# Kernel tuning notes

Hardware: AMD Instinct MI355X
Metric: run time of the kernel (lower is better)

The kernel has to match this reference:

```python
import jax, jax.numpy as jnp
import numpy as np

INV_SQRT2 = 0.7071067811865476
SCALES = 3


def dwt_analysis(x, dec_lo, dec_hi, scales):
    """Multi-level 1D DWT along last axis (pywt/ptwt convention).
    x: [B, D]. dec_lo/dec_hi are cross-correlation filters (torch conv1d
    semantics, i.e. the flipped pywt decomposition filters as stored by the
    repo). Returns [cA_s | cD_s | ... | cD_1] truncated to the last D columns
    (identity for Haar on power-of-two D)."""
    flen = dec_lo.shape[0]
    pad = (2 * flen - 3) // 2  # ptwt zero-pad; 0 for Haar (flen=2)
    filt = jnp.stack([dec_lo, dec_hi])[:, None, :]  # [2, 1, flen]
    lo = x[:, None, :]  # [B, 1, D]
    highs = []
    for _ in range(scales):
        out = jax.lax.conv_general_dilated(
            lo, filt, window_strides=(2,), padding=[(pad, pad)],
            dimension_numbers=('NCH', 'OIH', 'NCH'))  # [B, 2, D/2]
        lo = out[:, 0:1, :]
        highs.append(out[:, 1, :])
    coeffs = jnp.concatenate([lo[:, 0, :]] + highs[::-1], axis=-1)
    return coeffs[:, -x.shape[-1]:]


def setup_inputs() -> dict:
    key = jax.random.key(0)
    k1, k2, k3, k4, k5 = jax.random.split(key, 5)
    B, D = 4096, 4096
    x = jax.random.normal(k1, (B, D), jnp.float32)
    diag_s = jax.random.normal(k2, (D,), jnp.float32)
    diag_g = jax.random.normal(k3, (D,), jnp.float32)
    diag_b = jax.random.normal(k4, (D,), jnp.float32)
    perm = jax.random.permutation(k5, jnp.arange(D))  # random column permutation
    # Haar analysis filters in cross-correlation (torch conv1d) orientation
    dec_lo = jnp.array([INV_SQRT2, INV_SQRT2], jnp.float32)
    dec_hi = jnp.array([INV_SQRT2, -INV_SQRT2], jnp.float32)
    return {"x": x, "diag_s": diag_s, "diag_g": diag_g, "diag_b": diag_b,
            "dec_lo": dec_lo, "dec_hi": dec_hi, "perm": perm, "scales": SCALES}


def reference(x, diag_s, diag_g, diag_b, dec_lo, dec_hi, perm, scales):
    # mul_b: x @ diag(b) == columnwise scale (same math, no O(d^2) matmul)
    h = x * diag_b
    h = dwt_analysis(h, dec_lo, dec_hi, scales)
    # mul_p: x @ P for a permutation matrix == column gather
    h = jnp.take(h, perm, axis=1)
    h = h * diag_g  # mul_g
    h = dwt_analysis(h, dec_lo, dec_hi, scales)
    return h * diag_s  # mul_s
```

## Files before the change

### kernel.cpp

```cpp
#include <hip/hip_runtime.h>


#define D   4096
#define NT  256
#define R   4

#define C_INV_SQRT2 0.70710678118654752440f

typedef float vf2 __attribute__((ext_vector_type(2)));
typedef float vf4 __attribute__((ext_vector_type(4)));

static __device__ __forceinline__ int swz(int i) {
    return i ^ ((i >> 5) & 31);
}

static __device__ __forceinline__ void dwt3_reg(const float v[16],
                                                float a3[2], float d3[2],
                                                float d2[4], float d1[8]) {
    float a1[8];
    #pragma unroll
    for (int j = 0; j < 8; ++j) {
        a1[j] = (v[2 * j] + v[2 * j + 1]) * C_INV_SQRT2;
        d1[j] = (v[2 * j] - v[2 * j + 1]) * C_INV_SQRT2;
    }
    float a2[4];
    #pragma unroll
    for (int j = 0; j < 4; ++j) {
        a2[j] = (a1[2 * j] + a1[2 * j + 1]) * C_INV_SQRT2;
        d2[j] = (a1[2 * j] - a1[2 * j + 1]) * C_INV_SQRT2;
    }
    #pragma unroll
    for (int j = 0; j < 2; ++j) {
        a3[j] = (a2[2 * j] + a2[2 * j + 1]) * C_INV_SQRT2;
        d3[j] = (a2[2 * j] - a2[2 * j + 1]) * C_INV_SQRT2;
    }
}

__global__ __launch_bounds__(NT) void wavelet_rows_kernel(
    const float* __restrict__ x,
    const float* __restrict__ diag_s,
    const float* __restrict__ diag_g,
    const float* __restrict__ diag_b,
    const int*   __restrict__ perm,
    float*       __restrict__ out)
{
    __shared__ float buf[D];

    const int t = threadIdx.x;
    const size_t row0 = (size_t)blockIdx.x * R;

    float db[16], dg[16];
    int   pidx[16];
    {
        const vf4* b4 = (const vf4*)diag_b;
        const vf4* g4 = (const vf4*)diag_g;
        const int4* p4 = (const int4*)perm;
        #pragma unroll
        for (int k = 0; k < 4; ++k) {
            vf4 bv = b4[4 * t + k];
            db[4 * k + 0] = bv.x; db[4 * k + 1] = bv.y;
            db[4 * k + 2] = bv.z; db[4 * k + 3] = bv.w;
            vf4 gv = g4[4 * t + k];
            dg[4 * k + 0] = gv.x; dg[4 * k + 1] = gv.y;
            dg[4 * k + 2] = gv.z; dg[4 * k + 3] = gv.w;
            int4 pv = p4[4 * t + k];
            pidx[4 * k + 0] = pv.x; pidx[4 * k + 1] = pv.y;
            pidx[4 * k + 2] = pv.z; pidx[4 * k + 3] = pv.w;
        }
    }

    vf4 xv[4];
    {
        const vf4* x4 = (const vf4*)(x + row0 * (size_t)D);
        #pragma unroll
        for (int k = 0; k < 4; ++k) xv[k] = x4[4 * t + k];
    }

    for (int r = 0; r < R; ++r) {
        float v[16];
        #pragma unroll
        for (int k = 0; k < 4; ++k) {
            v[4 * k + 0] = xv[k].x * db[4 * k + 0];
            v[4 * k + 1] = xv[k].y * db[4 * k + 1];
            v[4 * k + 2] = xv[k].z * db[4 * k + 2];
            v[4 * k + 3] = xv[k].w * db[4 * k + 3];
        }

        if (r + 1 < R) {
            const vf4* xn = (const vf4*)(x + (row0 + r + 1) * (size_t)D);
            #pragma unroll
            for (int k = 0; k < 4; ++k) xv[k] = xn[4 * t + k];
        }

        float a3[2], d3[2], d2[4], d1[8];
        dwt3_reg(v, a3, d3, d2, d1);

        #pragma unroll
        for (int j = 0; j < 2; ++j) buf[swz(2 * t + j)]        = a3[j];
        #pragma unroll
        for (int j = 0; j < 2; ++j) buf[swz(512 + 2 * t + j)]  = d3[j];
        #pragma unroll
        for (int j = 0; j < 4; ++j) buf[swz(1024 + 4 * t + j)] = d2[j];
        #pragma unroll
        for (int j = 0; j < 8; ++j) buf[swz(2048 + 8 * t + j)] = d1[j];

        __syncthreads();

        float w[16];
        #pragma unroll
        for (int k = 0; k < 16; ++k) {
            w[k] = buf[swz(pidx[k])] * dg[k];
        }

        __syncthreads();

        float b3[2], e3[2], e2[4], e1[8];
        dwt3_reg(w, b3, e3, e2, e1);

        float* orow = out + (row0 + r) * (size_t)D;
        {
            const vf2* s2 = (const vf2*)diag_s;
            vf2* o2 = (vf2*)orow;
            vf2 sv, ov;
            sv = s2[t];
            ov.x = b3[0] * sv.x; ov.y = b3[1] * sv.y;
            o2[t] = ov;
            sv = s2[256 + t];
            ov.x = e3[0] * sv.x; ov.y = e3[1] * sv.y;
            o2[256 + t] = ov;

            const vf4* s4 = (const vf4*)diag_s;
            vf4* o4 = (vf4*)orow;
            vf4 sw, o;
            sw = s4[256 + t];
            o.x = e2[0] * sw.x; o.y = e2[1] * sw.y;
            o.z = e2[2] * sw.z; o.w = e2[3] * sw.w;
            o4[256 + t] = o;
            sw = s4[512 + 2 * t];
            o.x = e1[0] * sw.x; o.y = e1[1] * sw.y;
            o.z = e1[2] * sw.z; o.w = e1[3] * sw.w;
            o4[512 + 2 * t] = o;
            sw = s4[512 + 2 * t + 1];
            o.x = e1[4] * sw.x; o.y = e1[5] * sw.y;
            o.z = e1[6] * sw.z; o.w = e1[7] * sw.w;
            o4[512 + 2 * t + 1] = o;
        }
    }
}

extern "C" void kernel_launch(void* const* d_in, const int* in_sizes, int n_in,
                              void* d_out, int out_size, void* d_ws, size_t ws_size,
                              hipStream_t stream) {
    const float* x      = (const float*)d_in[0];
    const float* diag_s = (const float*)d_in[1];
    const float* diag_g = (const float*)d_in[2];
    const float* diag_b = (const float*)d_in[3];
    const int* perm     = (const int*)d_in[6];
    float* out          = (float*)d_out;

    const int B = 4096 / R;
    wavelet_rows_kernel<<<B, NT, 0, stream>>>(x, diag_s, diag_g, diag_b, perm, out);
}
```

Baseline: 131.7 us.

## Interleave four rows per LDS slot as vf4 to batch the permutation gather

Each block now loads all four rows up front and runs the first DWT on every row. It then stores the coefficients interleaved as one vf4 per column in a 64 KB LDS array, so the permutation gather becomes one 16-byte LDS read per column for all four rows. This replaces four per-row rounds of scalar LDS writes and gathers, and their eight barriers, with a single barrier. The cost is much higher register pressure from holding 4x16 values plus the inputs, and 64 KB of LDS per block, which limits occupancy. The swizzle is changed to suit 16-byte elements.

```diff
diff --git a/kernel.cpp b/kernel.cpp
--- a/kernel.cpp
+++ b/kernel.cpp
@@ -10,29 +10,27 @@
 typedef float vf2 __attribute__((ext_vector_type(2)));
 typedef float vf4 __attribute__((ext_vector_type(4)));
 
-static __device__ __forceinline__ int swz(int i) {
-    return i ^ ((i >> 5) & 31);
+static __device__ __forceinline__ int swzB(int p) {
+    return p ^ ((p >> 3) & 7);
 }
 
-static __device__ __forceinline__ void dwt3_reg(const float v[16],
-                                                float a3[2], float d3[2],
-                                                float d2[4], float d1[8]) {
+static __device__ __forceinline__ void dwt3_reg(const float v[16], float c[16]) {
     float a1[8];
     #pragma unroll
     for (int j = 0; j < 8; ++j) {
-        a1[j] = (v[2 * j] + v[2 * j + 1]) * C_INV_SQRT2;
-        d1[j] = (v[2 * j] - v[2 * j + 1]) * C_INV_SQRT2;
+        a1[j]     = (v[2 * j] + v[2 * j + 1]) * C_INV_SQRT2;
+        c[8 + j]  = (v[2 * j] - v[2 * j + 1]) * C_INV_SQRT2;
     }
     float a2[4];
     #pragma unroll
     for (int j = 0; j < 4; ++j) {
-        a2[j] = (a1[2 * j] + a1[2 * j + 1]) * C_INV_SQRT2;
-        d2[j] = (a1[2 * j] - a1[2 * j + 1]) * C_INV_SQRT2;
+        a2[j]    = (a1[2 * j] + a1[2 * j + 1]) * C_INV_SQRT2;
+        c[4 + j] = (a1[2 * j] - a1[2 * j + 1]) * C_INV_SQRT2;
     }
     #pragma unroll
     for (int j = 0; j < 2; ++j) {
-        a3[j] = (a2[2 * j] + a2[2 * j + 1]) * C_INV_SQRT2;
-        d3[j] = (a2[2 * j] - a2[2 * j + 1]) * C_INV_SQRT2;
+        c[j]     = (a2[2 * j] + a2[2 * j + 1]) * C_INV_SQRT2;
+        c[2 + j] = (a2[2 * j] - a2[2 * j + 1]) * C_INV_SQRT2;
     }
 }
 
@@ -44,7 +42,7 @@
     const int*   __restrict__ perm,
     float*       __restrict__ out)
 {
-    __shared__ float buf[D];
+    __shared__ vf4 lds4[D];
 
     const int t = threadIdx.x;
     const size_t row0 = (size_t)blockIdx.x * R;
@@ -69,82 +67,89 @@
         }
     }
 
-    vf4 xv[4];
-    {
-        const vf4* x4 = (const vf4*)(x + row0 * (size_t)D);
+    int pos[16];
+    #pragma unroll
+    for (int j = 0; j < 2; ++j) pos[j]     = 2 * t + j;
+    #pragma unroll
+    for (int j = 0; j < 2; ++j) pos[2 + j] = 512 + 2 * t + j;
+    #pragma unroll
+    for (int j = 0; j < 4; ++j) pos[4 + j] = 1024 + 4 * t + j;
+    #pragma unroll
+    for (int j = 0; j < 8; ++j) pos[8 + j] = 2048 + 8 * t + j;
+
+    vf4 xv[R][4];
+    #pragma unroll
+    for (int r = 0; r < R; ++r) {
+        const vf4* x4 = (const vf4*)(x + (row0 + r) * (size_t)D);
         #pragma unroll
-        for (int k = 0; k < 4; ++k) xv[k] = x4[4 * t + k];
+        for (int k = 0; k < 4; ++k) xv[r][k] = x4[4 * t + k];
     }
 
+    float cf[R][16];
+    #pragma unroll
     for (int r = 0; r < R; ++r) {
         float v[16];
         #pragma unroll
         for (int k = 0; k < 4; ++k) {
-            v[4 * k + 0] = xv[k].x * db[4 * k + 0];
-            v[4 * k + 1] = xv[k].y * db[4 * k + 1];
-            v[4 * k + 2] = xv[k].z * db[4 * k + 2];
-            v[4 * k + 3] = xv[k].w * db[4 * k + 3];
+            v[4 * k + 0] = xv[r][k].x * db[4 * k + 0];
+            v[4 * k + 1] = xv[r][k].y * db[4 * k + 1];
+            v[4 * k + 2] = xv[r][k].z * db[4 * k + 2];
+            v[4 * k + 3] = xv[r][k].w * db[4 * k + 3];
         }
+        dwt3_reg(v, cf[r]);
+    }
 
-        if (r + 1 < R) {
-            const vf4* xn = (const vf4*)(x + (row0 + r + 1) * (size_t)D);
-            #pragma unroll
-            for (int k = 0; k < 4; ++k) xv[k] = xn[4 * t + k];
-        }
+    #pragma unroll
+    for (int k = 0; k < 16; ++k) {
+        vf4 c4;
+        c4.x = cf[0][k]; c4.y = cf[1][k];
+        c4.z = cf[2][k]; c4.w = cf[3][k];
+        lds4[swzB(pos[k])] = c4;
+    }
 
-        float a3[2], d3[2], d2[4], d1[8];
-        dwt3_reg(v, a3, d3, d2, d1);
+    __syncthreads();
 
-        #pragma unroll
-        for (int j = 0; j < 2; ++j) buf[swz(2 * t + j)]        = a3[j];
-        #pragma unroll
-        for (int j = 0; j < 2; ++j) buf[swz(512 + 2 * t + j)]  = d3[j];
-        #pragma unroll
-        for (int j = 0; j < 4; ++j) buf[swz(1024 + 4 * t + j)] = d2[j];
-        #pragma unroll
-        for (int j = 0; j < 8; ++j) buf[swz(2048 + 8 * t + j)] = d1[j];
+    float w[R][16];
+    #pragma unroll
+    for (int k = 0; k < 16; ++k) {
+        vf4 f = lds4[swzB(pidx[k])];
+        w[0][k] = f.x * dg[k];
+        w[1][k] = f.y * dg[k];
+        w[2][k] = f.z * dg[k];
+        w[3][k] = f.w * dg[k];
+    }
 
-        __syncthreads();
+    const vf2* s2 = (const vf2*)diag_s;
+    const vf4* s4 = (const vf4*)diag_s;
+    const vf2 sA   = s2[t];
+    const vf2 sD3  = s2[256 + t];
+    const vf4 sD2  = s4[256 + t];
+    const vf4 sD1a = s4[512 + 2 * t];
+    const vf4 sD1b = s4[512 + 2 * t + 1];
 
-        float w[16];
-        #pragma unroll
-        for (int k = 0; k < 16; ++k) {
-            w[k] = buf[swz(pidx[k])] * dg[k];
-        }
-
-        __syncthreads();
-
-        float b3[2], e3[2], e2[4], e1[8];
-        dwt3_reg(w, b3, e3, e2, e1);
+    #pragma unroll
+    for (int r = 0; r < R; ++r) {
+        float e[16];
+        dwt3_reg(w[r], e);
 
         float* orow = out + (row0 + r) * (size_t)D;
-        {
-            const vf2* s2 = (const vf2*)diag_s;
-            vf2* o2 = (vf2*)orow;
-            vf2 sv, ov;
-            sv = s2[t];
-            ov.x = b3[0] * sv.x; ov.y = b3[1] * sv.y;
-            o2[t] = ov;
-            sv = s2[256 + t];
-            ov.x = e3[0] * sv.x; ov.y = e3[1] * sv.y;
-            o2[256 + t] = ov;
-
-            const vf4* s4 = (const vf4*)diag_s;
-            vf4* o4 = (vf4*)orow;
-            vf4 sw, o;
-            sw = s4[256 + t];
-            o.x = e2[0] * sw.x; o.y = e2[1] * sw.y;
-            o.z = e2[2] * sw.z; o.w = e2[3] * sw.w;
-            o4[256 + t] = o;
-            sw = s4[512 + 2 * t];
-            o.x = e1[0] * sw.x; o.y = e1[1] * sw.y;
-            o.z = e1[2] * sw.z; o.w = e1[3] * sw.w;
-            o4[512 + 2 * t] = o;
-            sw = s4[512 + 2 * t + 1];
-            o.x = e1[4] * sw.x; o.y = e1[5] * sw.y;
-            o.z = e1[6] * sw.z; o.w = e1[7] * sw.w;
-            o4[512 + 2 * t + 1] = o;
-        }
+        vf2* o2 = (vf2*)orow;
+        vf4* o4 = (vf4*)orow;
+        vf2 ov;
+        ov.x = e[0] * sA.x;  ov.y = e[1] * sA.y;
+        o2[t] = ov;
+        ov.x = e[2] * sD3.x; ov.y = e[3] * sD3.y;
+        o2[256 + t] = ov;
+        vf4 o;
+        o.x = e[4] * sD2.x; o.y = e[5] * sD2.y;
+        o.z = e[6] * sD2.z; o.w = e[7] * sD2.w;
+        o4[256 + t] = o;
+        o.x = e[8]  * sD1a.x; o.y = e[9]  * sD1a.y;
+        o.z = e[10] * sD1a.z; o.w = e[11] * sD1a.w;
+        o4[512 + 2 * t] = o;
+        o.x = e[12] * sD1b.x; o.y = e[13] * sD1b.y;
+        o.z = e[14] * sD1b.z; o.w = e[15] * sD1b.w;
+        o4[512 + 2 * t + 1] = o;
     }
 }
 
```

Result: no change. 131.3 us (-0.3%).
